# Optimization experiments

Measured on AMD Instinct MI355X. Metric: run time of the kernel, lower is better.

## Reference

```python
import jax, jax.numpy as jnp
import numpy as np

N = 50000
F_IN = 128
HID = 16
CLS = 40
NEG_SLOPE = 0.2


def gat_layer(x, src, dst, W, a_src, a_dst, b, heads, out_ch):
    # x: [N, Fin]; src/dst: [E] (self-loops included); W: [Fin, heads*out_ch]
    n = x.shape[0]
    h = (x @ W).reshape(n, heads, out_ch)                    # [N, H, C]
    al_s = jnp.einsum('nhc,hc->nh', h, a_src)                # [N, H]
    al_d = jnp.einsum('nhc,hc->nh', h, a_dst)                # [N, H]
    e = jax.nn.leaky_relu(al_s[src] + al_d[dst], NEG_SLOPE)  # [E, H]
    # segment softmax over incoming edges of each dst node
    m = jax.ops.segment_max(e, dst, num_segments=n)          # [N, H]
    ex = jnp.exp(e - m[dst])
    den = jax.ops.segment_sum(ex, dst, num_segments=n)
    alpha = ex / den[dst]                                    # [E, H]
    out = jax.ops.segment_sum(h[src] * alpha[:, :, None], dst, num_segments=n)
    return out.reshape(n, heads * out_ch) + b


def setup_inputs() -> dict:
    key = jax.random.key(0)
    ks = jax.random.split(key, 16)
    E = 800000
    x = jax.random.normal(ks[0], (N, F_IN), dtype=jnp.float32)
    edge_index = jax.random.randint(ks[1], (2, E), 0, N, dtype=jnp.int64)
    s = 0.1
    W1 = jax.random.normal(ks[2], (F_IN, 7 * HID), dtype=jnp.float32) * s
    a_src1 = jax.random.normal(ks[3], (7, HID), dtype=jnp.float32) * s
    a_dst1 = jax.random.normal(ks[4], (7, HID), dtype=jnp.float32) * s
    b1 = jnp.zeros((7 * HID,), dtype=jnp.float32)
    W2 = jax.random.normal(ks[5], (7 * HID, 6 * HID), dtype=jnp.float32) * s
    a_src2 = jax.random.normal(ks[6], (6, HID), dtype=jnp.float32) * s
    a_dst2 = jax.random.normal(ks[7], (6, HID), dtype=jnp.float32) * s
    b2 = jnp.zeros((6 * HID,), dtype=jnp.float32)
    W3 = jax.random.normal(ks[8], (6 * HID, 6 * CLS), dtype=jnp.float32) * s
    a_src3 = jax.random.normal(ks[9], (6, CLS), dtype=jnp.float32) * s
    a_dst3 = jax.random.normal(ks[10], (6, CLS), dtype=jnp.float32) * s
    b3 = jnp.zeros((6 * CLS,), dtype=jnp.float32)
    return {
        'x': x, 'edge_index': edge_index,
        'W1': W1, 'a_src1': a_src1, 'a_dst1': a_dst1, 'b1': b1,
        'W2': W2, 'a_src2': a_src2, 'a_dst2': a_dst2, 'b2': b2,
        'W3': W3, 'a_src3': a_src3, 'a_dst3': a_dst3, 'b3': b3,
    }


def reference(x, edge_index, W1, a_src1, a_dst1, b1, W2, a_src2, a_dst2, b2, W3, a_src3, a_dst3, b3):
    # add self-loops once (PyG GATConv default add_self_loops=True)
    loops = jnp.arange(N, dtype=edge_index.dtype)
    src = jnp.concatenate([edge_index[0], loops])
    dst = jnp.concatenate([edge_index[1], loops])
    # dropout layers are identity in eval mode
    h = gat_layer(x, src, dst, W1, a_src1, a_dst1, b1, 7, HID)
    h = jax.nn.relu(h)
    h = gat_layer(h, src, dst, W2, a_src2, a_dst2, b2, 6, HID)
    h = jax.nn.relu(h)
    out = gat_layer(h, src, dst, W3, a_src3, a_dst3, b3, 6, CLS)
    return out
```

## Files before the change

kernel.cpp:

```cpp
#include <hip/hip_runtime.h>
#include <hip/hip_fp16.h>
#include <cstdint>

#define NNODES 50000

__device__ inline void wave_lds_fence() {
  asm volatile("s_waitcnt lgkmcnt(0)" ::: "memory");
  __builtin_amdgcn_wave_barrier();
}

__global__ void hist_kernel(const int* __restrict__ ei, int E, int Nn, int* __restrict__ cnt) {
  int i = blockIdx.x * blockDim.x + threadIdx.x;
  int ET = E + Nn;
  if (i >= ET) return;
  int d = (i < E) ? ei[E + i] : (i - E);
  atomicAdd(&cnt[d], 1);
}

__global__ void scan1_kernel(const int* __restrict__ in, int n, int* __restrict__ incl,
                             int* __restrict__ bsum) {
  __shared__ int sd[256];
  int g = blockIdx.x * 256 + threadIdx.x;
  int v = (g < n) ? in[g] : 0;
  sd[threadIdx.x] = v;
  __syncthreads();
  for (int off = 1; off < 256; off <<= 1) {
    int t = (threadIdx.x >= off) ? sd[threadIdx.x - off] : 0;
    __syncthreads();
    sd[threadIdx.x] += t;
    __syncthreads();
  }
  if (g < n) incl[g] = sd[threadIdx.x];
  if (threadIdx.x == 255) bsum[blockIdx.x] = sd[255];
}

__global__ void scan3_kernel(const int* __restrict__ incl, const int* __restrict__ bscan,
                             int n, int* __restrict__ rowptr) {
  int g = blockIdx.x * 256 + threadIdx.x;
  if (g == 0) rowptr[0] = 0;
  if (g < n) {
    int off = (blockIdx.x > 0) ? bscan[blockIdx.x - 1] : 0;
    rowptr[g + 1] = incl[g] + off;
  }
}

__global__ void scatter_kernel(const int* __restrict__ ei, int E, int Nn,
                               const int* __restrict__ rowptr, int* __restrict__ cnt2,
                               int* __restrict__ esorted) {
  int i = blockIdx.x * blockDim.x + threadIdx.x;
  int ET = E + Nn;
  if (i >= ET) return;
  int s, d;
  if (i < E) { s = ei[i]; d = ei[E + i]; }
  else       { s = i - E; d = i - E; }
  int pos = rowptr[d] + atomicAdd(&cnt2[d], 1);
  esorted[pos] = s;
}

template <int FIN, int HC, int BLOCK>
__global__ __launch_bounds__(BLOCK) void gemm_kernel(const float* __restrict__ X,
                                                     const float* __restrict__ W,
                                                     __half* __restrict__ Hout) {
  constexpr int NT = 16;
  constexpr int TM = 4, TN = 4;
  constexpr int CG = HC / TN;
  __shared__ __align__(16) float xs[FIN * NT];
  const int n0 = blockIdx.x * NT;
  for (int i = threadIdx.x * 4; i < NT * FIN; i += BLOCK * 4) {
    float4 v = *(const float4*)(X + (size_t)n0 * FIN + i);
    int node = i / FIN, k = i % FIN;
    xs[(k + 0) * NT + node] = v.x;
    xs[(k + 1) * NT + node] = v.y;
    xs[(k + 2) * NT + node] = v.z;
    xs[(k + 3) * NT + node] = v.w;
  }
  __syncthreads();
  const int cg = threadIdx.x % CG;
  const int ng = threadIdx.x / CG;
  if (ng >= NT / TM) return;
  const int c0 = cg * TN;
  const int i0 = ng * TM;
  float acc[TM][TN];
#pragma unroll
  for (int i = 0; i < TM; ++i)
#pragma unroll
    for (int j = 0; j < TN; ++j) acc[i][j] = 0.f;
#pragma unroll 4
  for (int k = 0; k < FIN; ++k) {
    const float4 wv = *(const float4*)(W + (size_t)k * HC + c0);
    const float4 xv = *(const float4*)(xs + k * NT + i0);
    acc[0][0] += xv.x * wv.x; acc[0][1] += xv.x * wv.y; acc[0][2] += xv.x * wv.z; acc[0][3] += xv.x * wv.w;
    acc[1][0] += xv.y * wv.x; acc[1][1] += xv.y * wv.y; acc[1][2] += xv.y * wv.z; acc[1][3] += xv.y * wv.w;
    acc[2][0] += xv.z * wv.x; acc[2][1] += xv.z * wv.y; acc[2][2] += xv.z * wv.z; acc[2][3] += xv.z * wv.w;
    acc[3][0] += xv.w * wv.x; acc[3][1] += xv.w * wv.y; acc[3][2] += xv.w * wv.z; acc[3][3] += xv.w * wv.w;
  }
#pragma unroll
  for (int i = 0; i < TM; ++i) {
    union { __half2 h2[2]; uint2 u; } pk;
    pk.h2[0] = __floats2half2_rn(acc[i][0], acc[i][1]);
    pk.h2[1] = __floats2half2_rn(acc[i][2], acc[i][3]);
    *(uint2*)(Hout + (size_t)(n0 + i0 + i) * HC + c0) = pk.u;
  }
}

template <int H, int C>
__global__ void alpha_kernel(const __half* __restrict__ Hbuf, const float* __restrict__ a_s,
                             const float* __restrict__ a_d, float* __restrict__ als8,
                             float* __restrict__ ald8, int n_nodes) {
  int i = blockIdx.x * blockDim.x + threadIdx.x;
  if (i >= n_nodes * H) return;
  int n = i / H, h = i % H;
  const __half2* hp = (const __half2*)(Hbuf + (size_t)n * H * C + (size_t)h * C);
  float s1 = 0.f, s2 = 0.f;
#pragma unroll
  for (int c = 0; c < C / 2; ++c) {
    float2 f = __half22float2(hp[c]);
    s1 += f.x * a_s[h * C + 2 * c] + f.y * a_s[h * C + 2 * c + 1];
    s2 += f.x * a_d[h * C + 2 * c] + f.y * a_d[h * C + 2 * c + 1];
  }
  als8[n * 8 + h] = s1;
  ald8[n * 8 + h] = s2;
}

template <int H, int C, int RELU>
__global__ __launch_bounds__(256) void agg_kernel(const __half* __restrict__ Hbuf,
                                                  const float* __restrict__ als8,
                                                  const float* __restrict__ ald8,
                                                  const int* __restrict__ rowptr,
                                                  const int* __restrict__ esrc,
                                                  const float* __restrict__ bias,
                                                  float* __restrict__ Out, int n_nodes) {
  constexpr int HC = H * C;
  constexpr int PAIRS = HC / 2;
  constexpr int CPL = (PAIRS + 63) / 64;
  constexpr int CP2 = C / 2;
  constexpr int UN = (CPL == 1) ? 8 : 4;
  const int wave = threadIdx.x >> 6;
  const int lane = threadIdx.x & 63;
  const int n = blockIdx.x * 4 + wave;
  __shared__ float s_w[4][64 * H];
  __shared__ int s_src[4][64];
  if (n >= n_nodes) return;

  const int e0 = rowptr[n];
  const int e1 = rowptr[n + 1];

  float aldn[H];
#pragma unroll
  for (int h = 0; h < H; ++h) aldn[h] = ald8[n * 8 + h];

  int pj[CPL], hd[CPL];
#pragma unroll
  for (int j = 0; j < CPL; ++j) { pj[j] = lane + 64 * j; hd[j] = pj[j] / CP2; }

  float acc0[CPL], acc1[CPL], lsum[CPL];
#pragma unroll
  for (int j = 0; j < CPL; ++j) { acc0[j] = 0.f; acc1[j] = 0.f; lsum[j] = 0.f; }

  for (int base = e0; base < e1; base += 64) {
    const int cnt = (e1 - base < 64) ? (e1 - base) : 64;
    int sreg = 0;
    if (lane < cnt) sreg = esrc[base + lane];
    s_src[wave][lane] = sreg;
    if (lane < cnt) {
      const float4 qa = *(const float4*)(als8 + (size_t)sreg * 8);
      const float4 qb = *(const float4*)(als8 + (size_t)sreg * 8 + 4);
      const float q[8] = {qa.x, qa.y, qa.z, qa.w, qb.x, qb.y, qb.z, qb.w};
#pragma unroll
      for (int h = 0; h < H; ++h) {
        float v = q[h] + aldn[h];
        v = v > 0.f ? v : 0.2f * v;
        s_w[wave][lane * H + h] = __expf(v);
      }
    } else {
#pragma unroll
      for (int h = 0; h < H; ++h) s_w[wave][lane * H + h] = 0.f;
    }
    wave_lds_fence();
    for (int t = 0; t < cnt; t += UN) {
      const __half* pp[UN];
#pragma unroll
      for (int k = 0; k < UN; ++k) pp[k] = Hbuf + (size_t)s_src[wave][t + k] * HC;
      __half2 f[UN][CPL];
#pragma unroll
      for (int k = 0; k < UN; ++k)
#pragma unroll
        for (int j = 0; j < CPL; ++j)
          if (pj[j] < PAIRS) f[k][j] = *(const __half2*)(pp[k] + 2 * pj[j]);
      float w[UN][CPL];
#pragma unroll
      for (int k = 0; k < UN; ++k)
#pragma unroll
        for (int j = 0; j < CPL; ++j)
          if (pj[j] < PAIRS) w[k][j] = s_w[wave][(t + k) * H + hd[j]];
#pragma unroll
      for (int k = 0; k < UN; ++k)
#pragma unroll
        for (int j = 0; j < CPL; ++j)
          if (pj[j] < PAIRS) {
            float2 ff = __half22float2(f[k][j]);
            lsum[j] += w[k][j];
            acc0[j] += w[k][j] * ff.x;
            acc1[j] += w[k][j] * ff.y;
          }
    }
    wave_lds_fence();
  }
#pragma unroll
  for (int j = 0; j < CPL; ++j) {
    if (pj[j] < PAIRS) {
      float inv = 1.f / lsum[j];
      float2 bv = *(const float2*)(bias + 2 * pj[j]);
      float o0 = acc0[j] * inv + bv.x;
      float o1 = acc1[j] * inv + bv.y;
      if (RELU) { o0 = fmaxf(o0, 0.f); o1 = fmaxf(o1, 0.f); }
      float2 o; o.x = o0; o.y = o1;
      *(float2*)(Out + (size_t)n * HC + 2 * pj[j]) = o;
    }
  }
}

extern "C" void kernel_launch(void* const* d_in, const int* in_sizes, int n_in,
                              void* d_out, int out_size, void* d_ws, size_t ws_size,
                              hipStream_t stream) {
  const int N = NNODES;
  const float* x  = (const float*)d_in[0];
  const int* ei   = (const int*)d_in[1];
  const float* W1 = (const float*)d_in[2];
  const float* as1 = (const float*)d_in[3];
  const float* ad1 = (const float*)d_in[4];
  const float* b1  = (const float*)d_in[5];
  const float* W2  = (const float*)d_in[6];
  const float* as2 = (const float*)d_in[7];
  const float* ad2 = (const float*)d_in[8];
  const float* b2  = (const float*)d_in[9];
  const float* W3  = (const float*)d_in[10];
  const float* as3 = (const float*)d_in[11];
  const float* ad3 = (const float*)d_in[12];
  const float* b3  = (const float*)d_in[13];
  float* out = (float*)d_out;
  const int E = in_sizes[1] / 2;
  const int ET = E + N;

  char* ws = (char*)d_ws;
  size_t off = 0;
  auto alloc = [&](size_t bytes) -> char* {
    char* p = ws + off;
    off += (bytes + 255) & ~(size_t)255;
    return p;
  };
  int* cnt     = (int*)alloc((size_t)N * 4);
  int* cnt2    = (int*)alloc((size_t)N * 4);
  int* incl    = (int*)alloc((size_t)N * 4);
  int* bsum    = (int*)alloc(512 * 4);
  int* bscan   = (int*)alloc(256 * 4);
  int* rowptr  = (int*)alloc((size_t)(N + 1) * 4);
  int* esorted = (int*)alloc((size_t)ET * 4);
  float* als   = (float*)alloc((size_t)N * 8 * 4);
  float* ald   = (float*)alloc((size_t)N * 8 * 4);
  __half* hbuf = (__half*)alloc((size_t)N * 240 * 2);
  float* abuf  = (float*)alloc((size_t)N * 112 * 4);

  hipMemsetAsync(cnt, 0, (size_t)N * 4, stream);
  hipMemsetAsync(cnt2, 0, (size_t)N * 4, stream);

  const int B1 = (N + 255) / 256;
  hist_kernel<<<(ET + 255) / 256, 256, 0, stream>>>(ei, E, N, cnt);
  scan1_kernel<<<B1, 256, 0, stream>>>(cnt, N, incl, bsum);
  scan1_kernel<<<1, 256, 0, stream>>>(bsum, B1, bscan, bsum + 256);
  scan3_kernel<<<B1, 256, 0, stream>>>(incl, bscan, N, rowptr);
  scatter_kernel<<<(ET + 255) / 256, 256, 0, stream>>>(ei, E, N, rowptr, cnt2, esorted);

  gemm_kernel<128, 112, 128><<<N / 16, 128, 0, stream>>>(x, W1, hbuf);
  alpha_kernel<7, 16><<<(N * 7 + 255) / 256, 256, 0, stream>>>(hbuf, as1, ad1, als, ald, N);
  agg_kernel<7, 16, 1><<<(N + 3) / 4, 256, 0, stream>>>(hbuf, als, ald, rowptr, esorted, b1, abuf, N);
  gemm_kernel<112, 96, 128><<<N / 16, 128, 0, stream>>>(abuf, W2, hbuf);
  alpha_kernel<6, 16><<<(N * 6 + 255) / 256, 256, 0, stream>>>(hbuf, as2, ad2, als, ald, N);
  agg_kernel<6, 16, 1><<<(N + 3) / 4, 256, 0, stream>>>(hbuf, als, ald, rowptr, esorted, b2, abuf, N);
  gemm_kernel<96, 240, 256><<<N / 16, 256, 0, stream>>>(abuf, W3, hbuf);
  alpha_kernel<6, 40><<<(N * 6 + 255) / 256, 256, 0, stream>>>(hbuf, as3, ad3, als, ald, N);
  agg_kernel<6, 40, 0><<<(N + 3) / 4, 256, 0, stream>>>(hbuf, als, ald, rowptr, esorted, b3, out, N);
}
```

Measured before the change: 472.5 us.

## Split wave into edge groups with 16-byte feature loads in aggregation

Restructures the aggregation kernel so each wave is divided into groups of lanes. Each group handles a different edge at the same time, and each lane loads 8 half-precision features at once as a uint4 instead of a half2. The per-group partial sums are combined at the end with xor shuffles, and the shared arrays are padded so unrolled reads past the edge count hit zeros. The aim is more memory-level parallelism and fewer, wider gather loads for small feature widths. The cost is extra cross-lane reduction work and some idle lanes when the feature width is not a multiple of the group size.

Result: no change. 479.3 us (+1.5%).

```diff
diff --git a/kernel.cpp b/kernel.cpp
--- a/kernel.cpp
+++ b/kernel.cpp
@@ -131,16 +131,22 @@
                                                   const float* __restrict__ bias,
                                                   float* __restrict__ Out, int n_nodes) {
   constexpr int HC = H * C;
-  constexpr int PAIRS = HC / 2;
-  constexpr int CPL = (PAIRS + 63) / 64;
-  constexpr int CP2 = C / 2;
-  constexpr int UN = (CPL == 1) ? 8 : 4;
+  constexpr int NCHUNK = HC / 8;
+  constexpr int GROUPS = (NCHUNK <= 16) ? 4 : 2;
+  constexpr int LPG = 64 / GROUPS;
+  constexpr int UN = 3;
+  constexpr int TPAD = 72;
   const int wave = threadIdx.x >> 6;
   const int lane = threadIdx.x & 63;
+  const int grp = lane / LPG;
+  const int lg = lane % LPG;
   const int n = blockIdx.x * 4 + wave;
-  __shared__ float s_w[4][64 * H];
-  __shared__ int s_src[4][64];
+  __shared__ float s_w[4][TPAD * H];
+  __shared__ int s_src[4][TPAD];
   if (n >= n_nodes) return;
+
+  if (lane < TPAD - 64) s_src[wave][64 + lane] = 0;
+  for (int z = lane; z < (TPAD - 64) * H; z += 64) s_w[wave][64 * H + z] = 0.f;
 
   const int e0 = rowptr[n];
   const int e1 = rowptr[n + 1];
@@ -149,13 +155,13 @@
 #pragma unroll
   for (int h = 0; h < H; ++h) aldn[h] = ald8[n * 8 + h];
 
-  int pj[CPL], hd[CPL];
-#pragma unroll
-  for (int j = 0; j < CPL; ++j) { pj[j] = lane + 64 * j; hd[j] = pj[j] / CP2; }
-
-  float acc0[CPL], acc1[CPL], lsum[CPL];
-#pragma unroll
-  for (int j = 0; j < CPL; ++j) { acc0[j] = 0.f; acc1[j] = 0.f; lsum[j] = 0.f; }
+  const int head = min((lg * 8) / C, H - 1);
+  const bool act = lg < NCHUNK;
+
+  float acc[8];
+  float lsum = 0.f;
+#pragma unroll
+  for (int j = 0; j < 8; ++j) acc[j] = 0.f;
 
   for (int base = e0; base < e1; base += 64) {
     const int cnt = (e1 - base < 64) ? (e1 - base) : 64;
@@ -177,46 +183,62 @@
       for (int h = 0; h < H; ++h) s_w[wave][lane * H + h] = 0.f;
     }
     wave_lds_fence();
-    for (int t = 0; t < cnt; t += UN) {
-      const __half* pp[UN];
-#pragma unroll
-      for (int k = 0; k < UN; ++k) pp[k] = Hbuf + (size_t)s_src[wave][t + k] * HC;
-      __half2 f[UN][CPL];
+    const int nit = (cnt + GROUPS - 1) / GROUPS;
+    for (int i = 0; i < nit; i += UN) {
+      int tt[UN], si[UN];
+      uint4 v[UN];
+      float w[UN];
+#pragma unroll
+      for (int k = 0; k < UN; ++k) tt[k] = (i + k) * GROUPS + grp;
+#pragma unroll
+      for (int k = 0; k < UN; ++k) si[k] = s_src[wave][tt[k]];
 #pragma unroll
       for (int k = 0; k < UN; ++k)
-#pragma unroll
-        for (int j = 0; j < CPL; ++j)
-          if (pj[j] < PAIRS) f[k][j] = *(const __half2*)(pp[k] + 2 * pj[j]);
-      float w[UN][CPL];
+        if (act) v[k] = *(const uint4*)(Hbuf + (size_t)si[k] * HC + lg * 8);
+#pragma unroll
+      for (int k = 0; k < UN; ++k) w[k] = s_w[wave][tt[k] * H + head];
 #pragma unroll
       for (int k = 0; k < UN; ++k)
-#pragma unroll
-        for (int j = 0; j < CPL; ++j)
-          if (pj[j] < PAIRS) w[k][j] = s_w[wave][(t + k) * H + hd[j]];
-#pragma unroll
-      for (int k = 0; k < UN; ++k)
-#pragma unroll
-        for (int j = 0; j < CPL; ++j)
-          if (pj[j] < PAIRS) {
-            float2 ff = __half22float2(f[k][j]);
-            lsum[j] += w[k][j];
-            acc0[j] += w[k][j] * ff.x;
-            acc1[j] += w[k][j] * ff.y;
-          }
+        if (act) {
+          const __half2* hp = (const __half2*)&v[k];
+          float2 f0 = __half22float2(hp[0]);
+          float2 f1 = __half22float2(hp[1]);
+          float2 f2 = __half22float2(hp[2]);
+          float2 f3 = __half22float2(hp[3]);
+          lsum += w[k];
+          acc[0] += w[k] * f0.x; acc[1] += w[k] * f0.y;
+          acc[2] += w[k] * f1.x; acc[3] += w[k] * f1.y;
+          acc[4] += w[k] * f2.x; acc[5] += w[k] * f2.y;
+          acc[6] += w[k] * f3.x; acc[7] += w[k] * f3.y;
+        }
     }
     wave_lds_fence();
   }
-#pragma unroll
-  for (int j = 0; j < CPL; ++j) {
-    if (pj[j] < PAIRS) {
-      float inv = 1.f / lsum[j];
-      float2 bv = *(const float2*)(bias + 2 * pj[j]);
-      float o0 = acc0[j] * inv + bv.x;
-      float o1 = acc1[j] * inv + bv.y;
-      if (RELU) { o0 = fmaxf(o0, 0.f); o1 = fmaxf(o1, 0.f); }
-      float2 o; o.x = o0; o.y = o1;
-      *(float2*)(Out + (size_t)n * HC + 2 * pj[j]) = o;
+
+#pragma unroll
+  for (int off = LPG; off < 64; off <<= 1) {
+    lsum += __shfl_xor(lsum, off);
+#pragma unroll
+    for (int j = 0; j < 8; ++j) acc[j] += __shfl_xor(acc[j], off);
+  }
+
+  if (grp == 0 && act) {
+    const float inv = 1.f / lsum;
+    const float4 b0 = *(const float4*)(bias + lg * 8);
+    const float4 b1 = *(const float4*)(bias + lg * 8 + 4);
+    float4 o0, o1;
+    o0.x = acc[0] * inv + b0.x; o0.y = acc[1] * inv + b0.y;
+    o0.z = acc[2] * inv + b0.z; o0.w = acc[3] * inv + b0.w;
+    o1.x = acc[4] * inv + b1.x; o1.y = acc[5] * inv + b1.y;
+    o1.z = acc[6] * inv + b1.z; o1.w = acc[7] * inv + b1.w;
+    if (RELU) {
+      o0.x = fmaxf(o0.x, 0.f); o0.y = fmaxf(o0.y, 0.f);
+      o0.z = fmaxf(o0.z, 0.f); o0.w = fmaxf(o0.w, 0.f);
+      o1.x = fmaxf(o1.x, 0.f); o1.y = fmaxf(o1.y, 0.f);
+      o1.z = fmaxf(o1.z, 0.f); o1.w = fmaxf(o1.w, 0.f);
     }
+    *(float4*)(Out + (size_t)n * HC + lg * 8) = o0;
+    *(float4*)(Out + (size_t)n * HC + lg * 8 + 4) = o1;
   }
 }
 
```
